# Optimization experiments

Measured on AMD Instinct MI355X. Metric: run time of the kernel, lower is better.

Reference implementation:

```python
import jax, jax.numpy as jnp
import numpy as np

N, NFEAT, NHID, NCLASS, NHEAD = 8192, 512, 64, 16, 4
ALPHA = 0.1  # leaky relu slope
NEG = -9e15


def setup_inputs() -> dict:
    key = jax.random.key(0)
    ks = jax.random.split(key, 7)
    x = jax.random.normal(ks[0], (N, NFEAT), dtype=jnp.float32)
    adj = (jax.random.uniform(ks[1], (N, N)) < 0.05).astype(jnp.float32)
    # per-head params: W [H, nfeat, nhid], a [H, 2*nhid] (xavier-ish scale)
    W = jax.random.normal(ks[2], (NHEAD, NFEAT, NHID), dtype=jnp.float32) * (1.0 / np.sqrt(NFEAT))
    a = jax.random.normal(ks[3], (NHEAD, 2 * NHID), dtype=jnp.float32) * (1.0 / np.sqrt(NHID))
    W_out = jax.random.normal(ks[4], (NHEAD * NHID, NCLASS), dtype=jnp.float32) * (1.0 / np.sqrt(NHEAD * NHID))
    a_out = jax.random.normal(ks[5], (2 * NCLASS,), dtype=jnp.float32) * (1.0 / np.sqrt(NCLASS))
    return {"x": x, "adj": adj, "W": W, "a": a, "W_out": W_out, "a_out": a_out}


def _gat_layer(h, adj, Wk, ak):
    """Dense pyGAT GraphAttentionLayer (eval mode, dropout = identity)."""
    d = Wk.shape[1]
    Wh = h @ Wk                         # [N, d]
    f1 = Wh @ ak[:d]                    # [N]
    f2 = Wh @ ak[d:]                    # [N]
    e = jax.nn.leaky_relu(f1[:, None] + f2[None, :], negative_slope=ALPHA)  # [N, N]
    att = jax.nn.softmax(jnp.where(adj > 0, e, NEG), axis=1)
    return att @ Wh                     # [N, d]


def reference(x, adj, W, a, W_out, a_out):
    # eval mode: F.dropout is identity
    heads = jax.vmap(lambda Wk, ak: jax.nn.elu(_gat_layer(x, adj, Wk, ak)))(W, a)  # [H, N, nhid]
    h = jnp.transpose(heads, (1, 0, 2)).reshape(x.shape[0], -1)                    # [N, H*nhid]
    out = jax.nn.elu(_gat_layer(h, adj, W_out, a_out))                             # [N, nclass]
    return jax.nn.log_softmax(out, axis=1)
```

## Files before the change

### kernel.cpp

```cpp
#include <hip/hip_runtime.h>
#include <hip/hip_bf16.h>

#define NN 8192
#define NFEAT 512
#define NHID 64
#define NCLASS 16
#define NHEAD 4
#define ALPHA 0.1f
#define CAP 768

typedef short bf16x8 __attribute__((ext_vector_type(8)));
typedef float f32x4 __attribute__((ext_vector_type(4)));

__device__ __forceinline__ float lrelu(float x) { return fmaxf(x, ALPHA * x); }
__device__ __forceinline__ float elu(float x) { return x > 0.f ? x : __expf(x) - 1.f; }
__device__ __forceinline__ short f2b(float x) {
  union { __bf16 b; short s; } c; c.b = (__bf16)x; return c.s;
}
__device__ __forceinline__ float b2f(short x) {
  union { unsigned int u; float f; } c; c.u = ((unsigned int)(unsigned short)x) << 16; return c.f;
}

#define UPF(w, v, A0, A1)                                  \
  {                                                        \
    const float lo_ = __uint_as_float((v) << 16);          \
    const float hi_ = __uint_as_float((v) & 0xffff0000u);  \
    (A0) += (w) * lo_;                                     \
    (A1) += (w) * hi_;                                     \
  }

__global__ __launch_bounds__(256) void k_xcvt(const float* __restrict__ x,
                                              short* __restrict__ xB) {
  const float4* x4 = reinterpret_cast<const float4*>(x);
  ushort4* o4 = reinterpret_cast<ushort4*>(xB);
  const int t0 = blockIdx.x * 256 + threadIdx.x;
#pragma unroll
  for (int it = 0; it < 4; ++it) {
    const int g = it * 262144 + t0;
    const float4 v = x4[g];
    ushort4 o;
    o.x = (unsigned short)f2b(v.x);
    o.y = (unsigned short)f2b(v.y);
    o.z = (unsigned short)f2b(v.z);
    o.w = (unsigned short)f2b(v.w);
    o4[g] = o;
  }
}

__global__ __launch_bounds__(256) void k_wprep(const float* __restrict__ W,
                                               short* __restrict__ WB) {
  __shared__ float t[64][65];
  const int h = blockIdx.y;
  const int k0 = blockIdx.x * 64;
  const int tid = threadIdx.x;
#pragma unroll
  for (int it = 0; it < 16; ++it) {
    const int r = it * 4 + (tid >> 6), c = tid & 63;
    t[r][c] = W[((size_t)h * NFEAT + k0 + r) * NHID + c];
  }
  __syncthreads();
#pragma unroll
  for (int it = 0; it < 16; ++it) {
    const int d = it * 4 + (tid >> 6), k = tid & 63;
    WB[((size_t)h * NHID + d) * NFEAT + k0 + k] = f2b(t[k][d]);
  }
}

__global__ __launch_bounds__(256) void k_gemm1m(const short* __restrict__ xB,
                                                const short* __restrict__ WB,
                                                float* __restrict__ Wh) {
  const int h = blockIdx.y;
  const int bm = blockIdx.x * 64;
  const int wv = threadIdx.x >> 6, lane = threadIdx.x & 63;
  const int mr = lane & 15, kg = lane >> 4;
  f32x4 acc0 = {0.f, 0.f, 0.f, 0.f}, acc1 = acc0, acc2 = acc0, acc3 = acc0;
  const short* ap = xB + (size_t)(bm + wv * 16 + mr) * NFEAT + kg * 8;
  const short* bp = WB + ((size_t)h * NHID + mr) * NFEAT + kg * 8;
#pragma unroll 2
  for (int k0 = 0; k0 < NFEAT; k0 += 32) {
    const bf16x8 af = *reinterpret_cast<const bf16x8*>(ap);
    const bf16x8 b0 = *reinterpret_cast<const bf16x8*>(bp);
    const bf16x8 b1 = *reinterpret_cast<const bf16x8*>(bp + 16 * NFEAT);
    const bf16x8 b2 = *reinterpret_cast<const bf16x8*>(bp + 32 * NFEAT);
    const bf16x8 b3 = *reinterpret_cast<const bf16x8*>(bp + 48 * NFEAT);
    acc0 = __builtin_amdgcn_mfma_f32_16x16x32_bf16(af, b0, acc0, 0, 0, 0);
    acc1 = __builtin_amdgcn_mfma_f32_16x16x32_bf16(af, b1, acc1, 0, 0, 0);
    acc2 = __builtin_amdgcn_mfma_f32_16x16x32_bf16(af, b2, acc2, 0, 0, 0);
    acc3 = __builtin_amdgcn_mfma_f32_16x16x32_bf16(af, b3, acc3, 0, 0, 0);
    ap += 32; bp += 32;
  }
#pragma unroll
  for (int q = 0; q < 4; ++q) {
    float* wp = Wh + ((size_t)h * NN + bm + wv * 16 + kg * 4 + q) * NHID + mr;
    wp[0]  = acc0[q];
    wp[16] = acc1[q];
    wp[32] = acc2[q];
    wp[48] = acc3[q];
  }
}

__global__ __launch_bounds__(256) void k_f12(const float* __restrict__ Wh,
                                             const float* __restrict__ a,
                                             float* __restrict__ f1,
                                             float* __restrict__ f2i,
                                             short* __restrict__ WhB) {
  int wid = blockIdx.x * 4 + (threadIdx.x >> 6);
  int lane = threadIdx.x & 63;
  int h = wid >> 13;
  int i = wid & (NN - 1);
  float v = Wh[((size_t)h * NN + i) * NHID + lane];
  WhB[(size_t)i * (NHEAD * NHID) + h * NHID + lane] = f2b(v);
  float s1 = v * a[h * 2 * NHID + lane];
  float s2 = v * a[h * 2 * NHID + NHID + lane];
#pragma unroll
  for (int off = 32; off; off >>= 1) { s1 += __shfl_xor(s1, off); s2 += __shfl_xor(s2, off); }
  if (lane == 0) { f1[h * NN + i] = s1; f2i[(size_t)i * 4 + h] = s2; }
}

__global__ __launch_bounds__(256) void k_rmax(const float* __restrict__ src,
                                              float* __restrict__ dst, int n, int stride,
                                              int boff) {
  const float* p = src + (size_t)blockIdx.x * boff;
  float m = -1e30f;
  for (int k = threadIdx.x; k < n; k += 256) m = fmaxf(m, p[(size_t)k * stride]);
#pragma unroll
  for (int off = 32; off; off >>= 1) m = fmaxf(m, __shfl_xor(m, off));
  __shared__ float sm[4];
  if ((threadIdx.x & 63) == 0) sm[threadIdx.x >> 6] = m;
  __syncthreads();
  if (threadIdx.x == 0) dst[blockIdx.x] = fmaxf(fmaxf(sm[0], sm[1]), fmaxf(sm[2], sm[3]));
}

__global__ __launch_bounds__(256) void k_scan(const float* __restrict__ adj,
                                              unsigned int* __restrict__ bmask) {
  const float4* a4 = reinterpret_cast<const float4*>(adj);
  const int t0 = blockIdx.x * 256 + threadIdx.x;
#pragma unroll 4
  for (int it = 0; it < 32; ++it) {
    const int g = it * 524288 + t0;
    const float4 v = a4[g];
    unsigned int nv = (unsigned int)((v.x > 0.f) | ((v.y > 0.f) << 1) |
                                     ((v.z > 0.f) << 2) | ((v.w > 0.f) << 3))
                      << ((threadIdx.x & 7) * 4);
    nv |= __shfl_xor(nv, 1);
    nv |= __shfl_xor(nv, 2);
    nv |= __shfl_xor(nv, 4);
    if ((threadIdx.x & 7) == 0) bmask[g >> 3] = nv;
  }
}

__global__ __launch_bounds__(256) void k_attn1b(const unsigned int* __restrict__ bmask,
                                                const short* __restrict__ WhB,
                                                const float* __restrict__ f1,
                                                const float* __restrict__ f2i,
                                                const float* __restrict__ f2max,
                                                short* __restrict__ hcat) {
  __shared__ unsigned short idx[CAP];
  __shared__ unsigned short wlb[NHEAD][CAP];
  __shared__ float swp[4][NHEAD];
  __shared__ float sinv[NHEAD];
  __shared__ int cnt;
  const int i = blockIdx.x;
  const int tid = threadIdx.x;
  const int wv = tid >> 6, lane = tid & 63;
  if (tid == 0) cnt = 0;
  __syncthreads();

  {
    unsigned int word = bmask[(size_t)i * 256 + tid];
    const int c = __popc(word);
    if (c) {
      int base = atomicAdd(&cnt, c);
      const int j0 = tid * 32;
      while (word) {
        const int b = __ffs(word) - 1;
        word &= word - 1;
        if (base < CAP) idx[base++] = (unsigned short)(j0 + b);
      }
    }
  }
  __syncthreads();
  const int n = min(cnt, CAP);

  float f1r[NHEAD], mrow[NHEAD], sw[NHEAD] = {0.f, 0.f, 0.f, 0.f};
#pragma unroll
  for (int h = 0; h < NHEAD; ++h) {
    f1r[h] = f1[h * NN + i];
    mrow[h] = lrelu(f1r[h] + f2max[h]);
  }
  for (int k = tid; k < n; k += 256) {
    const int j = idx[k];
    const float4 f = *reinterpret_cast<const float4*>(f2i + (size_t)j * 4);
    const float w0 = __expf(lrelu(f1r[0] + f.x) - mrow[0]);
    const float w1 = __expf(lrelu(f1r[1] + f.y) - mrow[1]);
    const float w2 = __expf(lrelu(f1r[2] + f.z) - mrow[2]);
    const float w3 = __expf(lrelu(f1r[3] + f.w) - mrow[3]);
    wlb[0][k] = (unsigned short)f2b(w0);
    wlb[1][k] = (unsigned short)f2b(w1);
    wlb[2][k] = (unsigned short)f2b(w2);
    wlb[3][k] = (unsigned short)f2b(w3);
    sw[0] += w0; sw[1] += w1; sw[2] += w2; sw[3] += w3;
  }
#pragma unroll
  for (int off = 32; off; off >>= 1)
#pragma unroll
    for (int h = 0; h < NHEAD; ++h) sw[h] += __shfl_xor(sw[h], off);
  if (lane == 0) {
#pragma unroll
    for (int h = 0; h < NHEAD; ++h) swp[wv][h] = sw[h];
  }
  __syncthreads();
  if (tid < NHEAD) sinv[tid] = 1.f / (swp[0][tid] + swp[1][tid] + swp[2][tid] + swp[3][tid]);

  const int g = lane >> 3, l = lane & 7;
  float acc[8] = {};
  const short* wb = WhB + wv * 64 + l * 8;
#pragma unroll 2
  for (int k = g; k < n; k += 8) {
    const int j = idx[k];
    const float w = b2f((short)wlb[wv][k]);
    const uint4 e = *reinterpret_cast<const uint4*>(wb + (size_t)j * 256);
    UPF(w, e.x, acc[0], acc[1])
    UPF(w, e.y, acc[2], acc[3])
    UPF(w, e.z, acc[4], acc[5])
    UPF(w, e.w, acc[6], acc[7])
  }
  __syncthreads();
#pragma unroll
  for (int u = 0; u < 8; ++u) {
    acc[u] += __shfl_xor(acc[u], 8);
    acc[u] += __shfl_xor(acc[u], 16);
    acc[u] += __shfl_xor(acc[u], 32);
  }
  if (lane < 8) {
    const float iv = sinv[wv];
    bf16x8 o;
#pragma unroll
    for (int u = 0; u < 8; ++u) o[u] = f2b(elu(acc[u] * iv));
    *reinterpret_cast<bf16x8*>(hcat + (size_t)i * 256 + wv * 64 + lane * 8) = o;
  }
}

__global__ __launch_bounds__(256) void k_gemm2(const short* __restrict__ hcat,
                                               const float* __restrict__ Wout,
                                               const float* __restrict__ aout,
                                               short* __restrict__ Wh2B,
                                               float* __restrict__ f1o,
                                               float* __restrict__ f2o) {
  __shared__ float sW[NHEAD * NHID][NCLASS + 1];
  __shared__ float sh[16][NHEAD * NHID + 1];
  const int tid = threadIdx.x;
  const int r = tid >> 4, c = tid & 15;
  const int row = blockIdx.x * 16 + r;
  for (int u = tid; u < 256 * 16; u += 256) sW[u >> 4][u & 15] = Wout[u];
  for (int u = tid; u < 16 * 256; u += 256)
    sh[u >> 8][u & 255] = b2f(hcat[(size_t)(blockIdx.x * 16 + (u >> 8)) * 256 + (u & 255)]);
  __syncthreads();
  float acc = 0.f;
#pragma unroll 8
  for (int f = 0; f < 256; ++f) acc += sh[r][f] * sW[f][c];
  Wh2B[(size_t)row * NCLASS + c] = f2b(acc);
  float s1 = acc * aout[c];
  float s2 = acc * aout[NCLASS + c];
#pragma unroll
  for (int off = 8; off; off >>= 1) { s1 += __shfl_xor(s1, off); s2 += __shfl_xor(s2, off); }
  if (c == 0) { f1o[row] = s1; f2o[row] = s2; }
}

__global__ __launch_bounds__(256) void k_attn2(const unsigned int* __restrict__ bmask,
                                               const short* __restrict__ Wh2B,
                                               const float* __restrict__ f1o,
                                               const float* __restrict__ f2o,
                                               const float* __restrict__ f2omax,
                                               float* __restrict__ out) {
  __shared__ unsigned short idx[CAP];
  __shared__ float wl[CAP];
  __shared__ float red[4][NCLASS];
  __shared__ float swp[4];
  __shared__ float sinvs;
  __shared__ int cnt;
  const int i = blockIdx.x;
  const int tid = threadIdx.x;
  const int wv = tid >> 6, lane = tid & 63;
  if (tid == 0) cnt = 0;
  __syncthreads();

  {
    unsigned int word = bmask[(size_t)i * 256 + tid];
    const int c = __popc(word);
    if (c) {
      int base = atomicAdd(&cnt, c);
      const int j0 = tid * 32;
      while (word) {
        const int b = __ffs(word) - 1;
        word &= word - 1;
        if (base < CAP) idx[base++] = (unsigned short)(j0 + b);
      }
    }
  }
  __syncthreads();
  const int n = min(cnt, CAP);

  const float f1r = f1o[i];
  const float mrow = lrelu(f1r + f2omax[0]);
  float sw = 0.f;
  for (int k = tid; k < n; k += 256) {
    const int j = idx[k];
    const float w = __expf(lrelu(f1r + f2o[j]) - mrow);
    wl[k] = w;
    sw += w;
  }
#pragma unroll
  for (int off = 32; off; off >>= 1) sw += __shfl_xor(sw, off);
  if (lane == 0) swp[wv] = sw;
  __syncthreads();
  if (tid == 0) sinvs = 1.f / (swp[0] + swp[1] + swp[2] + swp[3]);

  const int g = tid >> 2, gl = tid & 3;
  float acc[4] = {};
  int k = g;
  int jc = (k < n) ? (int)idx[k] : -1;
  while (jc >= 0) {
    const int kn = k + 64;
    const int jn = (kn < n) ? (int)idx[kn] : -1;
    const float w = wl[k];
    const uint2 v = *reinterpret_cast<const uint2*>(Wh2B + (size_t)jc * NCLASS + gl * 4);
    UPF(w, v.x, acc[0], acc[1])
    UPF(w, v.y, acc[2], acc[3])
    k = kn; jc = jn;
  }
  __syncthreads();
#pragma unroll
  for (int u = 0; u < 4; ++u) {
    acc[u] += __shfl_xor(acc[u], 4);
    acc[u] += __shfl_xor(acc[u], 8);
    acc[u] += __shfl_xor(acc[u], 16);
    acc[u] += __shfl_xor(acc[u], 32);
  }
  if (lane < 4) {
#pragma unroll
    for (int u = 0; u < 4; ++u) red[wv][lane * 4 + u] = acc[u];
  }
  __syncthreads();
  if (tid < NCLASS) {
    const float s = red[0][tid] + red[1][tid] + red[2][tid] + red[3][tid];
    const float v = elu(s * sinvs);
    float vm = v;
#pragma unroll
    for (int off = 8; off; off >>= 1) vm = fmaxf(vm, __shfl_xor(vm, off, 16));
    float ex = __expf(v - vm);
#pragma unroll
    for (int off = 8; off; off >>= 1) ex += __shfl_xor(ex, off, 16);
    out[(size_t)i * NCLASS + tid] = v - vm - __logf(ex);
  }
}

extern "C" void kernel_launch(void* const* d_in, const int* in_sizes, int n_in,
                              void* d_out, int out_size, void* d_ws, size_t ws_size,
                              hipStream_t stream) {
  const float* x    = (const float*)d_in[0];
  const float* adj  = (const float*)d_in[1];
  const float* W    = (const float*)d_in[2];
  const float* a    = (const float*)d_in[3];
  const float* Wout = (const float*)d_in[4];
  const float* aout = (const float*)d_in[5];
  float* out = (float*)d_out;
  char* ws = (char*)d_ws;
  const size_t MB = 1048576;

  short* xB            = (short*)(ws);
  float* Wh            = (float*)(ws + 8 * MB);
  short* WhB           = (short*)(ws + 16 * MB);
  unsigned int* bmask  = (unsigned int*)(ws + 20 * MB);
  short* hcat          = (short*)(ws + 28 * MB);
  short* WB            = (short*)(ws + 32 * MB);
  float* f1            = (float*)(ws + 32 * MB + 262144);
  float* f2i           = (float*)(ws + 32 * MB + 393216);
  float* f1o           = (float*)(ws + 32 * MB + 524288);
  float* f2o           = (float*)(ws + 32 * MB + 557056);
  short* Wh2B          = (short*)(ws + 32 * MB + 589824);
  float* f2max         = (float*)(ws + 32 * MB + 851968);
  float* f2omax        = (float*)(ws + 32 * MB + 852032);

  k_xcvt<<<1024, 256, 0, stream>>>(x, xB);
  k_wprep<<<dim3(8, 4), 256, 0, stream>>>(W, WB);
  k_gemm1m<<<dim3(NN / 64, NHEAD), 256, 0, stream>>>(xB, WB, Wh);
  k_f12<<<NN * NHEAD / 4, 256, 0, stream>>>(Wh, a, f1, f2i, WhB);
  k_rmax<<<NHEAD, 256, 0, stream>>>(f2i, f2max, NN, 4, 1);
  k_scan<<<2048, 256, 0, stream>>>(adj, bmask);
  k_attn1b<<<NN, 256, 0, stream>>>(bmask, WhB, f1, f2i, f2max, hcat);
  k_gemm2<<<NN / 16, 256, 0, stream>>>(hcat, Wout, aout, Wh2B, f1o, f2o);
  k_rmax<<<1, 256, 0, stream>>>(f2o, f2omax, NN, 1, 0);
  k_attn2<<<NN, 256, 0, stream>>>(bmask, Wh2B, f1o, f2o, f2omax, out);
}
```

Measured before the change: 234.2 us.

## Fuse x conversion, GEMM1, f1/f2 epilogue and adjacency scan into one kernel

Removes the separate x-to-bf16 conversion kernel and makes GEMM1 convert fp32 x on the fly. The f1/f2 dot products and the bf16 WhB write move into the GEMM epilogue, written through a shared-memory tile. That GEMM is merged with the adjacency bitmask scan into one launch with disjoint block ranges, so the fp32 Wh round trip and several launches disappear. The attention kernels also pack the bf16 weight and the neighbour index into one 32-bit shared word and process two neighbours per iteration for more memory-level parallelism. GEMM1 now reads fp32 x, which is twice the bytes, and the GEMM blocks are scheduled after 2048 scan blocks.

```diff
diff --git a/kernel.cpp b/kernel.cpp
--- a/kernel.cpp
+++ b/kernel.cpp
@@ -29,24 +29,6 @@
     (A1) += (w) * hi_;                                     \
   }
 
-__global__ __launch_bounds__(256) void k_xcvt(const float* __restrict__ x,
-                                              short* __restrict__ xB) {
-  const float4* x4 = reinterpret_cast<const float4*>(x);
-  ushort4* o4 = reinterpret_cast<ushort4*>(xB);
-  const int t0 = blockIdx.x * 256 + threadIdx.x;
-#pragma unroll
-  for (int it = 0; it < 4; ++it) {
-    const int g = it * 262144 + t0;
-    const float4 v = x4[g];
-    ushort4 o;
-    o.x = (unsigned short)f2b(v.x);
-    o.y = (unsigned short)f2b(v.y);
-    o.z = (unsigned short)f2b(v.z);
-    o.w = (unsigned short)f2b(v.w);
-    o4[g] = o;
-  }
-}
-
 __global__ __launch_bounds__(256) void k_wprep(const float* __restrict__ W,
                                                short* __restrict__ WB) {
   __shared__ float t[64][65];
@@ -66,19 +48,48 @@
   }
 }
 
-__global__ __launch_bounds__(256) void k_gemm1m(const short* __restrict__ xB,
-                                                const short* __restrict__ WB,
-                                                float* __restrict__ Wh) {
-  const int h = blockIdx.y;
-  const int bm = blockIdx.x * 64;
-  const int wv = threadIdx.x >> 6, lane = threadIdx.x & 63;
+__global__ __launch_bounds__(256) void k_mega1(const float* __restrict__ adj,
+                                               unsigned int* __restrict__ bmask,
+                                               const float* __restrict__ x,
+                                               const short* __restrict__ WB,
+                                               const float* __restrict__ a,
+                                               short* __restrict__ WhB,
+                                               float* __restrict__ f1,
+                                               float* __restrict__ f2i) {
+  const int tid = threadIdx.x;
+  if (blockIdx.x < 2048) {
+    const float4* a4 = reinterpret_cast<const float4*>(adj);
+    const int t0 = blockIdx.x * 256 + tid;
+#pragma unroll 4
+    for (int it = 0; it < 32; ++it) {
+      const int g = it * 524288 + t0;
+      const float4 v = a4[g];
+      unsigned int nv = (unsigned int)((v.x > 0.f) | ((v.y > 0.f) << 1) |
+                                       ((v.z > 0.f) << 2) | ((v.w > 0.f) << 3))
+                        << ((tid & 7) * 4);
+      nv |= __shfl_xor(nv, 1);
+      nv |= __shfl_xor(nv, 2);
+      nv |= __shfl_xor(nv, 4);
+      if ((tid & 7) == 0) bmask[g >> 3] = nv;
+    }
+    return;
+  }
+  __shared__ short tile[64][72];
+  const int bid = blockIdx.x - 2048;
+  const int h = bid >> 7;
+  const int bm = (bid & 127) * 64;
+  const int wv = tid >> 6, lane = tid & 63;
   const int mr = lane & 15, kg = lane >> 4;
   f32x4 acc0 = {0.f, 0.f, 0.f, 0.f}, acc1 = acc0, acc2 = acc0, acc3 = acc0;
-  const short* ap = xB + (size_t)(bm + wv * 16 + mr) * NFEAT + kg * 8;
+  const float* ap = x + (size_t)(bm + wv * 16 + mr) * NFEAT + kg * 8;
   const short* bp = WB + ((size_t)h * NHID + mr) * NFEAT + kg * 8;
 #pragma unroll 2
   for (int k0 = 0; k0 < NFEAT; k0 += 32) {
-    const bf16x8 af = *reinterpret_cast<const bf16x8*>(ap);
+    const float4 xa = *reinterpret_cast<const float4*>(ap);
+    const float4 xb = *reinterpret_cast<const float4*>(ap + 4);
+    bf16x8 af;
+    af[0] = f2b(xa.x); af[1] = f2b(xa.y); af[2] = f2b(xa.z); af[3] = f2b(xa.w);
+    af[4] = f2b(xb.x); af[5] = f2b(xb.y); af[6] = f2b(xb.z); af[7] = f2b(xb.w);
     const bf16x8 b0 = *reinterpret_cast<const bf16x8*>(bp);
     const bf16x8 b1 = *reinterpret_cast<const bf16x8*>(bp + 16 * NFEAT);
     const bf16x8 b2 = *reinterpret_cast<const bf16x8*>(bp + 32 * NFEAT);
@@ -89,32 +100,48 @@
     acc3 = __builtin_amdgcn_mfma_f32_16x16x32_bf16(af, b3, acc3, 0, 0, 0);
     ap += 32; bp += 32;
   }
+  float a1v[4], a2v[4];
+#pragma unroll
+  for (int c = 0; c < 4; ++c) {
+    a1v[c] = a[h * 128 + mr + c * 16];
+    a2v[c] = a[h * 128 + 64 + mr + c * 16];
+  }
 #pragma unroll
   for (int q = 0; q < 4; ++q) {
-    float* wp = Wh + ((size_t)h * NN + bm + wv * 16 + kg * 4 + q) * NHID + mr;
-    wp[0]  = acc0[q];
-    wp[16] = acc1[q];
-    wp[32] = acc2[q];
-    wp[48] = acc3[q];
-  }
-}
-
-__global__ __launch_bounds__(256) void k_f12(const float* __restrict__ Wh,
-                                             const float* __restrict__ a,
-                                             float* __restrict__ f1,
-                                             float* __restrict__ f2i,
-                                             short* __restrict__ WhB) {
-  int wid = blockIdx.x * 4 + (threadIdx.x >> 6);
-  int lane = threadIdx.x & 63;
-  int h = wid >> 13;
-  int i = wid & (NN - 1);
-  float v = Wh[((size_t)h * NN + i) * NHID + lane];
-  WhB[(size_t)i * (NHEAD * NHID) + h * NHID + lane] = f2b(v);
-  float s1 = v * a[h * 2 * NHID + lane];
-  float s2 = v * a[h * 2 * NHID + NHID + lane];
-#pragma unroll
-  for (int off = 32; off; off >>= 1) { s1 += __shfl_xor(s1, off); s2 += __shfl_xor(s2, off); }
-  if (lane == 0) { f1[h * NN + i] = s1; f2i[(size_t)i * 4 + h] = s2; }
+    float s1 = acc0[q] * a1v[0] + acc1[q] * a1v[1] + acc2[q] * a1v[2] + acc3[q] * a1v[3];
+    float s2 = acc0[q] * a2v[0] + acc1[q] * a2v[1] + acc2[q] * a2v[2] + acc3[q] * a2v[3];
+#pragma unroll
+    for (int off = 1; off < 16; off <<= 1) {
+      s1 += __shfl_xor(s1, off);
+      s2 += __shfl_xor(s2, off);
+    }
+    if (mr == 0) {
+      const int i = bm + wv * 16 + kg * 4 + q;
+      f1[h * NN + i] = s1;
+      f2i[(size_t)i * 4 + h] = s2;
+    }
+  }
+#pragma unroll
+  for (int q = 0; q < 4; ++q) {
+    const int r = wv * 16 + kg * 4 + q;
+    tile[r][mr +  0] = f2b(acc0[q]);
+    tile[r][mr + 16] = f2b(acc1[q]);
+    tile[r][mr + 32] = f2b(acc2[q]);
+    tile[r][mr + 48] = f2b(acc3[q]);
+  }
+  __syncthreads();
+  {
+    const int row = tid >> 2, seg = tid & 3;
+    bf16x8 o0, o1;
+#pragma unroll
+    for (int u = 0; u < 8; ++u) {
+      o0[u] = tile[row][seg * 16 + u];
+      o1[u] = tile[row][seg * 16 + 8 + u];
+    }
+    short* dst = WhB + (size_t)(bm + row) * 256 + h * 64 + seg * 16;
+    *reinterpret_cast<bf16x8*>(dst) = o0;
+    *reinterpret_cast<bf16x8*>(dst + 8) = o1;
+  }
 }
 
 __global__ __launch_bounds__(256) void k_rmax(const float* __restrict__ src,
@@ -129,24 +156,6 @@
   if ((threadIdx.x & 63) == 0) sm[threadIdx.x >> 6] = m;
   __syncthreads();
   if (threadIdx.x == 0) dst[blockIdx.x] = fmaxf(fmaxf(sm[0], sm[1]), fmaxf(sm[2], sm[3]));
-}
-
-__global__ __launch_bounds__(256) void k_scan(const float* __restrict__ adj,
-                                              unsigned int* __restrict__ bmask) {
-  const float4* a4 = reinterpret_cast<const float4*>(adj);
-  const int t0 = blockIdx.x * 256 + threadIdx.x;
-#pragma unroll 4
-  for (int it = 0; it < 32; ++it) {
-    const int g = it * 524288 + t0;
-    const float4 v = a4[g];
-    unsigned int nv = (unsigned int)((v.x > 0.f) | ((v.y > 0.f) << 1) |
-                                     ((v.z > 0.f) << 2) | ((v.w > 0.f) << 3))
-                      << ((threadIdx.x & 7) * 4);
-    nv |= __shfl_xor(nv, 1);
-    nv |= __shfl_xor(nv, 2);
-    nv |= __shfl_xor(nv, 4);
-    if ((threadIdx.x & 7) == 0) bmask[g >> 3] = nv;
-  }
 }
 
 __global__ __launch_bounds__(256) void k_attn1b(const unsigned int* __restrict__ bmask,
@@ -156,7 +165,7 @@
                                                 const float* __restrict__ f2max,
                                                 short* __restrict__ hcat) {
   __shared__ unsigned short idx[CAP];
-  __shared__ unsigned short wlb[NHEAD][CAP];
+  __shared__ unsigned int widx[NHEAD][CAP];
   __shared__ float swp[4][NHEAD];
   __shared__ float sinv[NHEAD];
   __shared__ int cnt;
@@ -195,10 +204,10 @@
     const float w1 = __expf(lrelu(f1r[1] + f.y) - mrow[1]);
     const float w2 = __expf(lrelu(f1r[2] + f.z) - mrow[2]);
     const float w3 = __expf(lrelu(f1r[3] + f.w) - mrow[3]);
-    wlb[0][k] = (unsigned short)f2b(w0);
-    wlb[1][k] = (unsigned short)f2b(w1);
-    wlb[2][k] = (unsigned short)f2b(w2);
-    wlb[3][k] = (unsigned short)f2b(w3);
+    widx[0][k] = ((unsigned int)(unsigned short)f2b(w0) << 16) | (unsigned int)j;
+    widx[1][k] = ((unsigned int)(unsigned short)f2b(w1) << 16) | (unsigned int)j;
+    widx[2][k] = ((unsigned int)(unsigned short)f2b(w2) << 16) | (unsigned int)j;
+    widx[3][k] = ((unsigned int)(unsigned short)f2b(w3) << 16) | (unsigned int)j;
     sw[0] += w0; sw[1] += w1; sw[2] += w2; sw[3] += w3;
   }
 #pragma unroll
@@ -215,15 +224,26 @@
   const int g = lane >> 3, l = lane & 7;
   float acc[8] = {};
   const short* wb = WhB + wv * 64 + l * 8;
+  const unsigned int* wrow = widx[wv];
 #pragma unroll 2
-  for (int k = g; k < n; k += 8) {
-    const int j = idx[k];
-    const float w = b2f((short)wlb[wv][k]);
-    const uint4 e = *reinterpret_cast<const uint4*>(wb + (size_t)j * 256);
-    UPF(w, e.x, acc[0], acc[1])
-    UPF(w, e.y, acc[2], acc[3])
-    UPF(w, e.z, acc[4], acc[5])
-    UPF(w, e.w, acc[6], acc[7])
+  for (int k = g; k < n; k += 16) {
+    const unsigned int v0 = wrow[k];
+    const int k1 = k + 8;
+    const unsigned int v1 = (k1 < n) ? wrow[k1] : 0u;
+    const int j0 = v0 & 0xffffu;
+    const float w0 = __uint_as_float(v0 & 0xffff0000u);
+    const int j1 = v1 & 0xffffu;
+    const float w1 = __uint_as_float(v1 & 0xffff0000u);
+    const uint4 e0 = *reinterpret_cast<const uint4*>(wb + (size_t)j0 * 256);
+    const uint4 e1 = *reinterpret_cast<const uint4*>(wb + (size_t)j1 * 256);
+    UPF(w0, e0.x, acc[0], acc[1])
+    UPF(w0, e0.y, acc[2], acc[3])
+    UPF(w0, e0.z, acc[4], acc[5])
+    UPF(w0, e0.w, acc[6], acc[7])
+    UPF(w1, e1.x, acc[0], acc[1])
+    UPF(w1, e1.y, acc[2], acc[3])
+    UPF(w1, e1.z, acc[4], acc[5])
+    UPF(w1, e1.w, acc[6], acc[7])
   }
   __syncthreads();
 #pragma unroll
@@ -274,7 +294,7 @@
                                                const float* __restrict__ f2omax,
                                                float* __restrict__ out) {
   __shared__ unsigned short idx[CAP];
-  __shared__ float wl[CAP];
+  __shared__ unsigned int wj[CAP];
   __shared__ float red[4][NCLASS];
   __shared__ float swp[4];
   __shared__ float sinvs;
@@ -307,7 +327,7 @@
   for (int k = tid; k < n; k += 256) {
     const int j = idx[k];
     const float w = __expf(lrelu(f1r + f2o[j]) - mrow);
-    wl[k] = w;
+    wj[k] = ((unsigned int)(unsigned short)f2b(w) << 16) | (unsigned int)j;
     sw += w;
   }
 #pragma unroll
@@ -318,16 +338,20 @@
 
   const int g = tid >> 2, gl = tid & 3;
   float acc[4] = {};
-  int k = g;
-  int jc = (k < n) ? (int)idx[k] : -1;
-  while (jc >= 0) {
-    const int kn = k + 64;
-    const int jn = (kn < n) ? (int)idx[kn] : -1;
-    const float w = wl[k];
-    const uint2 v = *reinterpret_cast<const uint2*>(Wh2B + (size_t)jc * NCLASS + gl * 4);
-    UPF(w, v.x, acc[0], acc[1])
-    UPF(w, v.y, acc[2], acc[3])
-    k = kn; jc = jn;
+  for (int k = g; k < n; k += 128) {
+    const unsigned int v0 = wj[k];
+    const int k1 = k + 64;
+    const unsigned int v1 = (k1 < n) ? wj[k1] : 0u;
+    const int j0 = v0 & 0xffffu;
+    const float w0 = __uint_as_float(v0 & 0xffff0000u);
+    const int j1 = v1 & 0xffffu;
+    const float w1 = __uint_as_float(v1 & 0xffff0000u);
+    const uint2 e0 = *reinterpret_cast<const uint2*>(Wh2B + (size_t)j0 * NCLASS + gl * 4);
+    const uint2 e1 = *reinterpret_cast<const uint2*>(Wh2B + (size_t)j1 * NCLASS + gl * 4);
+    UPF(w0, e0.x, acc[0], acc[1])
+    UPF(w0, e0.y, acc[2], acc[3])
+    UPF(w1, e1.x, acc[0], acc[1])
+    UPF(w1, e1.y, acc[2], acc[3])
   }
   __syncthreads();
 #pragma unroll
@@ -368,26 +392,21 @@
   char* ws = (char*)d_ws;
   const size_t MB = 1048576;
 
-  short* xB            = (short*)(ws);
-  float* Wh            = (float*)(ws + 8 * MB);
-  short* WhB           = (short*)(ws + 16 * MB);
-  unsigned int* bmask  = (unsigned int*)(ws + 20 * MB);
-  short* hcat          = (short*)(ws + 28 * MB);
-  short* WB            = (short*)(ws + 32 * MB);
-  float* f1            = (float*)(ws + 32 * MB + 262144);
-  float* f2i           = (float*)(ws + 32 * MB + 393216);
-  float* f1o           = (float*)(ws + 32 * MB + 524288);
-  float* f2o           = (float*)(ws + 32 * MB + 557056);
-  short* Wh2B          = (short*)(ws + 32 * MB + 589824);
-  float* f2max         = (float*)(ws + 32 * MB + 851968);
-  float* f2omax        = (float*)(ws + 32 * MB + 852032);
-
-  k_xcvt<<<1024, 256, 0, stream>>>(x, xB);
+  unsigned int* bmask  = (unsigned int*)(ws);
+  short* WhB           = (short*)(ws + 8 * MB);
+  short* hcat          = (short*)(ws + 12 * MB);
+  short* WB            = (short*)(ws + 16 * MB);
+  float* f1            = (float*)(ws + 16 * MB + 262144);
+  float* f2i           = (float*)(ws + 16 * MB + 393216);
+  float* f1o           = (float*)(ws + 16 * MB + 524288);
+  float* f2o           = (float*)(ws + 16 * MB + 557056);
+  short* Wh2B          = (short*)(ws + 16 * MB + 589824);
+  float* f2max         = (float*)(ws + 16 * MB + 851968);
+  float* f2omax        = (float*)(ws + 16 * MB + 852032);
+
   k_wprep<<<dim3(8, 4), 256, 0, stream>>>(W, WB);
-  k_gemm1m<<<dim3(NN / 64, NHEAD), 256, 0, stream>>>(xB, WB, Wh);
-  k_f12<<<NN * NHEAD / 4, 256, 0, stream>>>(Wh, a, f1, f2i, WhB);
+  k_mega1<<<2048 + 512, 256, 0, stream>>>(adj, bmask, x, WB, a, WhB, f1, f2i);
   k_rmax<<<NHEAD, 256, 0, stream>>>(f2i, f2max, NN, 4, 1);
-  k_scan<<<2048, 256, 0, stream>>>(adj, bmask);
   k_attn1b<<<NN, 256, 0, stream>>>(bmask, WhB, f1, f2i, f2max, hcat);
   k_gemm2<<<NN / 16, 256, 0, stream>>>(hcat, Wout, aout, Wh2B, f1o, f2o);
   k_rmax<<<1, 256, 0, stream>>>(f2o, f2omax, NN, 1, 0);
```

After: 244.6 us, median of 2. 1.04x slower.
